# Performance work log

Hardware: AMD Instinct MI355X
Metric: run time of the kernel (lower is better)

## Reference

```python
import jax, jax.numpy as jnp
import numpy as np

VOCAB = 50000
EMB = 32
HID = 32
NUM_CLASSES = 2


def setup_inputs() -> dict:
    key = jax.random.key(0)
    ks = jax.random.split(key, 8)
    B, S = 1024, 512
    x = jax.random.randint(ks[0], (B, S), 0, VOCAB, dtype=jnp.int64)
    # embedding table has vocab_size + 1 rows, per `len(encoder.vocab) + 1`
    emb = jax.random.normal(ks[1], (VOCAB + 1, EMB), dtype=jnp.float32)
    s = 1.0 / np.sqrt(HID)
    w_ih = jax.random.uniform(ks[2], (4 * HID, EMB), jnp.float32, -s, s)
    w_hh = jax.random.uniform(ks[3], (4 * HID, HID), jnp.float32, -s, s)
    b_ih = jax.random.uniform(ks[4], (4 * HID,), jnp.float32, -s, s)
    b_hh = jax.random.uniform(ks[5], (4 * HID,), jnp.float32, -s, s)
    sf = 1.0 / np.sqrt(HID)
    fc_w = jax.random.uniform(ks[6], (NUM_CLASSES, HID), jnp.float32, -sf, sf)
    fc_b = jax.random.uniform(ks[7], (NUM_CLASSES,), jnp.float32, -sf, sf)
    return {"x": x, "emb": emb, "w_ih": w_ih, "w_hh": w_hh,
            "b_ih": b_ih, "b_hh": b_hh, "fc_w": fc_w, "fc_b": fc_b}


def _lstm_last_h(x, emb, w_ih, w_hh, b_ih, b_hh):
    xe = emb[x]                                        # [B, S, EMB]
    # precompute input-to-gate projection for all timesteps: [B, S, 4H]
    xp = jnp.einsum('bse,ge->bsg', xe, w_ih) + (b_ih + b_hh)
    B = x.shape[0]
    h0 = jnp.zeros((B, HID), xp.dtype)
    c0 = jnp.zeros((B, HID), xp.dtype)

    def step(carry, xt):
        h, c = carry
        gates = xt + h @ w_hh.T                        # [B, 4H]
        i, f, g, o = jnp.split(gates, 4, axis=-1)      # PyTorch gate order
        i = jax.nn.sigmoid(i)
        f = jax.nn.sigmoid(f)
        g = jnp.tanh(g)
        o = jax.nn.sigmoid(o)
        c = f * c + i * g
        h = o * jnp.tanh(c)
        return (h, c), None

    (h_n, c_n), _ = jax.lax.scan(step, (h0, c0), jnp.swapaxes(xp, 0, 1))
    return h_n                                          # last-timestep hidden


def reference(x, emb, w_ih, w_hh, b_ih, b_hh, fc_w, fc_b):
    h_last = _lstm_last_h(x, emb, w_ih, w_hh, b_ih, b_hh)
    return h_last @ fc_w.T + fc_b                       # [B, 2]
```

## Files before the change

kernel.cpp:

```cpp
#include <hip/hip_runtime.h>


#define LOG2E 1.44269504088896340736f

typedef float f32x2 __attribute__((ext_vector_type(2)));
typedef unsigned uv2 __attribute__((ext_vector_type(2)));
typedef float f32x16 __attribute__((ext_vector_type(16)));
typedef float f32x32 __attribute__((ext_vector_type(32)));

__device__ __forceinline__ float fast_rcp(float x) { return __builtin_amdgcn_rcpf(x); }
__device__ __forceinline__ float fast_exp2(float x) { return __builtin_amdgcn_exp2f(x); }

__device__ __forceinline__ f32x2 bcast_both(float x) {
    uv2 r = __builtin_amdgcn_permlane32_swap(__float_as_uint(x), __float_as_uint(x),
                                             false, false);
    f32x2 o;
    o.x = __uint_as_float(r.x);
    o.y = __uint_as_float(r.y);
    return o;
}

#define ROTA(V) __int_as_float(__builtin_amdgcn_mov_dpp(__float_as_int(V), 0x13C, 0xF, 0xF, true))
#define ROTB(V) __int_as_float(__builtin_amdgcn_mov_dpp(__float_as_int(V), 0x134, 0xF, 0xF, true))

__global__ __launch_bounds__(64, 1) void build_ptab(
    const float4* __restrict__ emb4, const float4* __restrict__ wih4,
    const float* __restrict__ bih, const float* __restrict__ bhh,
    float2* __restrict__ ptab, int nrows) {
    const int lane = threadIdx.x;

    float w0[32], w1[32];
#pragma unroll
    for (int q = 0; q < 8; ++q) {
        float4 a = wih4[lane * 8 + q];
        float4 b = wih4[(lane + 64) * 8 + q];
        w0[4 * q + 0] = a.x; w0[4 * q + 1] = a.y; w0[4 * q + 2] = a.z; w0[4 * q + 3] = a.w;
        w1[4 * q + 0] = b.x; w1[4 * q + 1] = b.y; w1[4 * q + 2] = b.z; w1[4 * q + 3] = b.w;
    }
    const float bias0 = bih[lane] + bhh[lane];
    const float bias1 = bih[lane + 64] + bhh[lane + 64];
    const float s0 = -LOG2E;
    const float s1 = (lane < 32) ? (2.0f * LOG2E) : (-LOG2E);

    for (int v = blockIdx.x; v < nrows; v += gridDim.x) {
        float a0 = bias0, a1 = bias1;
#pragma unroll
        for (int q = 0; q < 8; ++q) {
            float4 e = emb4[v * 8 + q];
            a0 = fmaf(e.x, w0[4 * q + 0], a0);
            a0 = fmaf(e.y, w0[4 * q + 1], a0);
            a0 = fmaf(e.z, w0[4 * q + 2], a0);
            a0 = fmaf(e.w, w0[4 * q + 3], a0);
            a1 = fmaf(e.x, w1[4 * q + 0], a1);
            a1 = fmaf(e.y, w1[4 * q + 1], a1);
            a1 = fmaf(e.z, w1[4 * q + 2], a1);
            a1 = fmaf(e.w, w1[4 * q + 3], a1);
        }
        ptab[v * 64 + lane] = make_float2(a0 * s0, a1 * s1);
    }
}

#define STEP(P)                                                                \
    do {                                                                       \
        float _a0 = fmaf(h, wI0, (P).x);                                       \
        float _b0 = fmaf(h, wI1, (P).y);                                       \
        float _a1 = 0.0f, _b1 = 0.0f;                                          \
        float _hA = h, _hB = h;                                                \
        _Pragma("unroll") for (int _j = 0; _j < 15; ++_j) {                    \
            _hA = ROTA(_hA);                                                   \
            _a0 = fmaf(_hA, wA0[_j], _a0);                                     \
            _b0 = fmaf(_hA, wA1[_j], _b0);                                     \
            _hB = ROTB(_hB);                                                   \
            _a1 = fmaf(_hB, wB0[_j], _a1);                                     \
            _b1 = fmaf(_hB, wB1[_j], _b1);                                     \
        }                                                                      \
        _hA = ROTA(_hA);                                                       \
        _a0 = fmaf(_hA, wA0[15], _a0);                                         \
        _b0 = fmaf(_hA, wA1[15], _b0);                                         \
        float _A0 = _a0 + _a1;                     \
        float _A1 = _b0 + _b1;                     \
        float _sg = fast_rcp(1.0f + fast_exp2(_A0));           \
        float _r1 = fast_rcp(1.0f + fast_exp2(_A1));           \
        f32x2 _bs = bcast_both(_sg);                \
        f32x2 _br = bcast_both(_r1);               \
        float _ggs = fmaf(-4.0f * LOG2E, _br.x, 2.0f * LOG2E);  \
        cs = fmaf(_bs.y, cs, _bs.x * _ggs);                                    \
        h = _br.y * fmaf(-2.0f, fast_rcp(1.0f + fast_exp2(cs)), 1.0f);         \
    } while (0)

template <bool PTAB>
__global__ __launch_bounds__(64)
__attribute__((amdgpu_waves_per_eu(1, 1)))
void lstm_scan(
    const int* __restrict__ x,
    const float2* __restrict__ ptab,
    const float* __restrict__ emb,
    const float* __restrict__ wih,
    const float* __restrict__ bih,
    const float* __restrict__ bhh,
    const float* __restrict__ whh,
    const float* __restrict__ fcw,
    const float* __restrict__ fcb,
    float* __restrict__ out,
    int S) {
    extern __shared__ int xrow[];
    const int b = blockIdx.x;
    const int lane = threadIdx.x;

    for (int i = lane; i < S + 16; i += 64) xrow[i] = (i < S) ? x[(size_t)b * S + i] : 0;
    __syncthreads();

    const float s0 = -LOG2E;
    const float s1 = (lane < 32) ? (2.0f * LOG2E) : (-LOG2E);

    int dirA, dirB;
    {
        int gA = __builtin_amdgcn_mov_dpp(lane, 0x13C, 0xF, 0xF, true);
        dirA = (gA == ((lane + 1) & 63)) ? 1 : -1;
        int gB = __builtin_amdgcn_mov_dpp(lane, 0x134, 0xF, 0xF, true);
        dirB = (gB == ((lane + 63) & 63)) ? -1 : 1;
    }

    float wI0, wI1;
    f32x16 wA0, wA1, wB0, wB1;
    {
        const int r0 = lane * 32;
        const int r1 = (lane + 64) * 32;
        wI0 = whh[r0 + (lane & 31)] * s0;
        wI1 = whh[r1 + (lane & 31)] * s1;
#pragma unroll
        for (int j = 0; j < 16; ++j) {
            int cA = (lane + dirA * (j + 1)) & 31;
            wA0[j] = whh[r0 + cA] * s0;
            wA1[j] = whh[r1 + cA] * s1;
        }
#pragma unroll
        for (int j = 0; j < 15; ++j) {
            int cB = (lane + dirB * (j + 1)) & 31;
            wB0[j] = whh[r0 + cB] * s0;
            wB1[j] = whh[r1 + cB] * s1;
        }
        wB0[15] = 0.0f;
        wB1[15] = 0.0f;
    }

    float h = 0.0f, cs = 0.0f;

    if constexpr (PTAB) {
        const char* pb = (const char*)ptab + (unsigned)(lane << 3);
        int i0 = xrow[4], i1 = xrow[5], i2 = xrow[6], i3 = xrow[7];
        f32x2 p0 = *(const f32x2*)(pb + ((unsigned)xrow[0] << 9));
        f32x2 p1 = *(const f32x2*)(pb + ((unsigned)xrow[1] << 9));
        f32x2 p2 = *(const f32x2*)(pb + ((unsigned)xrow[2] << 9));
        f32x2 p3 = *(const f32x2*)(pb + ((unsigned)xrow[3] << 9));
        int t = 0;
        for (; t + 8 <= S; t += 4) {
            STEP(p0); p0 = *(const f32x2*)(pb + ((unsigned)i0 << 9)); i0 = xrow[t + 8];
            STEP(p1); p1 = *(const f32x2*)(pb + ((unsigned)i1 << 9)); i1 = xrow[t + 9];
            STEP(p2); p2 = *(const f32x2*)(pb + ((unsigned)i2 << 9)); i2 = xrow[t + 10];
            STEP(p3); p3 = *(const f32x2*)(pb + ((unsigned)i3 << 9)); i3 = xrow[t + 11];
        }
        if (t + 0 < S) STEP(p0);
        if (t + 1 < S) STEP(p1);
        if (t + 2 < S) STEP(p2);
        if (t + 3 < S) STEP(p3);
        if (t + 4 < S) { f32x2 q = *(const f32x2*)(pb + ((unsigned)i0 << 9)); STEP(q); }
        if (t + 5 < S) { f32x2 q = *(const f32x2*)(pb + ((unsigned)i1 << 9)); STEP(q); }
        if (t + 6 < S) { f32x2 q = *(const f32x2*)(pb + ((unsigned)i2 << 9)); STEP(q); }
    } else {
        f32x32 wi0, wi1;
        {
            const float4* wih4 = (const float4*)wih;
#pragma unroll
            for (int q = 0; q < 8; ++q) {
                float4 a = wih4[lane * 8 + q];
                float4 bb = wih4[(lane + 64) * 8 + q];
                wi0[4 * q + 0] = a.x * s0; wi0[4 * q + 1] = a.y * s0;
                wi0[4 * q + 2] = a.z * s0; wi0[4 * q + 3] = a.w * s0;
                wi1[4 * q + 0] = bb.x * s1; wi1[4 * q + 1] = bb.y * s1;
                wi1[4 * q + 2] = bb.z * s1; wi1[4 * q + 3] = bb.w * s1;
            }
        }
        const float bias0 = (bih[lane] + bhh[lane]) * s0;
        const float bias1 = (bih[lane + 64] + bhh[lane + 64]) * s1;
        const float4* emb4 = (const float4*)emb;
        for (int t = 0; t < S; ++t) {
            int idx = xrow[t];
            float a0 = bias0, a1 = bias1;
#pragma unroll
            for (int q = 0; q < 8; ++q) {
                float4 e = emb4[(size_t)idx * 8 + q];
                a0 = fmaf(e.x, wi0[4 * q + 0], a0);
                a0 = fmaf(e.y, wi0[4 * q + 1], a0);
                a0 = fmaf(e.z, wi0[4 * q + 2], a0);
                a0 = fmaf(e.w, wi0[4 * q + 3], a0);
                a1 = fmaf(e.x, wi1[4 * q + 0], a1);
                a1 = fmaf(e.y, wi1[4 * q + 1], a1);
                a1 = fmaf(e.z, wi1[4 * q + 2], a1);
                a1 = fmaf(e.w, wi1[4 * q + 3], a1);
            }
            f32x2 _p; _p.x = a0; _p.y = a1;
            STEP(_p);
        }
    }

    float wv0 = fcw[lane & 31];
    float wv1 = fcw[32 + (lane & 31)];
    float p0v = (lane < 32) ? h * wv0 : 0.0f;
    float p1v = (lane < 32) ? h * wv1 : 0.0f;
#pragma unroll
    for (int m = 32; m >= 1; m >>= 1) {
        p0v += __shfl_xor(p0v, m, 64);
        p1v += __shfl_xor(p1v, m, 64);
    }
    if (lane == 0) {
        out[b * 2 + 0] = p0v + fcb[0];
        out[b * 2 + 1] = p1v + fcb[1];
    }
}

extern "C" void kernel_launch(void* const* d_in, const int* in_sizes, int n_in,
                              void* d_out, int out_size, void* d_ws, size_t ws_size,
                              hipStream_t stream) {
    const int* x = (const int*)d_in[0];
    const float* emb = (const float*)d_in[1];
    const float* wih = (const float*)d_in[2];
    const float* whh = (const float*)d_in[3];
    const float* bih = (const float*)d_in[4];
    const float* bhh = (const float*)d_in[5];
    const float* fcw = (const float*)d_in[6];
    const float* fcb = (const float*)d_in[7];
    float* out = (float*)d_out;

    const int B = out_size / 2;
    const int S = in_sizes[0] / B;
    const int nrows = in_sizes[1] / 32;

    const size_t need = (size_t)nrows * 64 * sizeof(float2);
    const size_t smem = (size_t)(S + 16) * sizeof(int);

    if (ws_size >= need) {
        float2* ptab = (float2*)d_ws;
        int nb = nrows < 8192 ? nrows : 8192;
        build_ptab<<<nb, 64, 0, stream>>>((const float4*)emb, (const float4*)wih,
                                          bih, bhh, ptab, nrows);
        lstm_scan<true><<<B, 64, smem, stream>>>(x, ptab, emb, wih, bih, bhh, whh,
                                                 fcw, fcb, out, S);
    } else {
        lstm_scan<false><<<B, 64, smem, stream>>>(x, nullptr, emb, wih, bih, bhh, whh,
                                                  fcw, fcb, out, S);
    }
}
```

Before: 138.6 us.

## Split hidden-state rotation into four shorter DPP chains using permlane16 swap

The recurrent matvec used two serial DPP rotation chains of about 16 steps each to gather the 32 hidden values. It now uses a permlane16 swap to fetch the value 16 lanes away and runs four interleaved rotation chains of about 8 steps each, with the weights rearranged to match. This shortens the serial dependency chain on the per-timestep critical path. In exchange it adds a cross-lane swap, more accumulators and registers, and a runtime check that works out which half of the swap result each lane should take.

```diff
diff --git a/kernel.cpp b/kernel.cpp
--- a/kernel.cpp
+++ b/kernel.cpp
@@ -5,7 +5,7 @@
 
 typedef float f32x2 __attribute__((ext_vector_type(2)));
 typedef unsigned uv2 __attribute__((ext_vector_type(2)));
-typedef float f32x16 __attribute__((ext_vector_type(16)));
+typedef float f32x8 __attribute__((ext_vector_type(8)));
 typedef float f32x32 __attribute__((ext_vector_type(32)));
 
 __device__ __forceinline__ float fast_rcp(float x) { return __builtin_amdgcn_rcpf(x); }
@@ -18,6 +18,18 @@
     o.x = __uint_as_float(r.x);
     o.y = __uint_as_float(r.y);
     return o;
+}
+
+__device__ __forceinline__ uv2 p16swap(unsigned x) {
+#if __has_builtin(__builtin_amdgcn_permlane16_swap)
+    return __builtin_amdgcn_permlane16_swap(x, x, false, false);
+#else
+    unsigned other = (unsigned)__shfl_xor((int)x, 16, 64);
+    uv2 r;
+    if (threadIdx.x & 16) { r.x = other; r.y = x; }
+    else                  { r.x = x;     r.y = other; }
+    return r;
+#endif
 }
 
 #define ROTA(V) __int_as_float(__builtin_amdgcn_mov_dpp(__float_as_int(V), 0x13C, 0xF, 0xF, true))
@@ -64,21 +76,28 @@
     do {                                                                       \
         float _a0 = fmaf(h, wI0, (P).x);                                       \
         float _b0 = fmaf(h, wI1, (P).y);                                       \
-        float _a1 = 0.0f, _b1 = 0.0f;                                          \
-        float _hA = h, _hB = h;                                                \
-        _Pragma("unroll") for (int _j = 0; _j < 15; ++_j) {                    \
+        uv2 _sw = p16swap(__float_as_uint(h));                                 \
+        float _h16 = __uint_as_float(useX ? _sw.x : _sw.y);                    \
+        float _a1 = 0.f, _b1 = 0.f, _a2 = 0.f, _b2 = 0.f, _a3 = 0.f, _b3 = 0.f;\
+        float _hA = h, _hB = h, _hC = _h16, _hD = _h16;                        \
+        _a0 = fmaf(_h16, C0[0], _a0);                                          \
+        _b0 = fmaf(_h16, C1[0], _b0);                                          \
+        _Pragma("unroll") for (int _j = 0; _j < 7; ++_j) {                     \
             _hA = ROTA(_hA);                                                   \
-            _a0 = fmaf(_hA, wA0[_j], _a0);                                     \
-            _b0 = fmaf(_hA, wA1[_j], _b0);                                     \
+            _a1 = fmaf(_hA, A0[_j], _a1); _b1 = fmaf(_hA, A1[_j], _b1);        \
             _hB = ROTB(_hB);                                                   \
-            _a1 = fmaf(_hB, wB0[_j], _a1);                                     \
-            _b1 = fmaf(_hB, wB1[_j], _b1);                                     \
+            _a2 = fmaf(_hB, B0[_j], _a2); _b2 = fmaf(_hB, B1[_j], _b2);        \
+            _hC = ROTA(_hC);                                                   \
+            _a0 = fmaf(_hC, C0[_j + 1], _a0); _b0 = fmaf(_hC, C1[_j + 1], _b0);\
+            _hD = ROTB(_hD);                                                   \
+            _a3 = fmaf(_hD, D0[_j], _a3); _b3 = fmaf(_hD, D1[_j], _b3);        \
         }                                                                      \
         _hA = ROTA(_hA);                                                       \
-        _a0 = fmaf(_hA, wA0[15], _a0);                                         \
-        _b0 = fmaf(_hA, wA1[15], _b0);                                         \
-        float _A0 = _a0 + _a1;                     \
-        float _A1 = _b0 + _b1;                     \
+        _a1 = fmaf(_hA, A0[7], _a1); _b1 = fmaf(_hA, A1[7], _b1);              \
+        _hB = ROTB(_hB);                                                       \
+        _a2 = fmaf(_hB, B0[7], _a2); _b2 = fmaf(_hB, B1[7], _b2);              \
+        float _A0 = (_a0 + _a1) + (_a2 + _a3);     \
+        float _A1 = (_b0 + _b1) + (_b2 + _b3);     \
         float _sg = fast_rcp(1.0f + fast_exp2(_A0));           \
         float _r1 = fast_rcp(1.0f + fast_exp2(_A1));           \
         f32x2 _bs = bcast_both(_sg);                \
@@ -120,28 +139,40 @@
         int gB = __builtin_amdgcn_mov_dpp(lane, 0x134, 0xF, 0xF, true);
         dirB = (gB == ((lane + 63) & 63)) ? -1 : 1;
     }
+    bool ok16;
+    {
+        uv2 t = p16swap((unsigned)lane);
+        ok16 = (t.x == (unsigned)(lane & ~16));
+    }
+    const bool useX = ((lane & 16) != 0) == ok16;
 
     float wI0, wI1;
-    f32x16 wA0, wA1, wB0, wB1;
+    f32x8 A0, A1, B0, B1, C0, C1, D0, D1;
     {
-        const int r0 = lane * 32;
-        const int r1 = (lane + 64) * 32;
-        wI0 = whh[r0 + (lane & 31)] * s0;
-        wI1 = whh[r1 + (lane & 31)] * s1;
-#pragma unroll
-        for (int j = 0; j < 16; ++j) {
+        const int r0w = lane * 32;
+        const int r1w = (lane + 64) * 32;
+        wI0 = whh[r0w + (lane & 31)] * s0;
+        wI1 = whh[r1w + (lane & 31)] * s1;
+#pragma unroll
+        for (int j = 0; j < 8; ++j) {
             int cA = (lane + dirA * (j + 1)) & 31;
-            wA0[j] = whh[r0 + cA] * s0;
-            wA1[j] = whh[r1 + cA] * s1;
-        }
-#pragma unroll
-        for (int j = 0; j < 15; ++j) {
             int cB = (lane + dirB * (j + 1)) & 31;
-            wB0[j] = whh[r0 + cB] * s0;
-            wB1[j] = whh[r1 + cB] * s1;
-        }
-        wB0[15] = 0.0f;
-        wB1[15] = 0.0f;
+            int cC = (lane + 16 + dirA * j) & 31;
+            A0[j] = whh[r0w + cA] * s0;
+            A1[j] = whh[r1w + cA] * s1;
+            B0[j] = whh[r0w + cB] * s0;
+            B1[j] = whh[r1w + cB] * s1;
+            C0[j] = whh[r0w + cC] * s0;
+            C1[j] = whh[r1w + cC] * s1;
+        }
+#pragma unroll
+        for (int k = 1; k < 8; ++k) {
+            int cD = (lane + 16 + dirB * k) & 31;
+            D0[k - 1] = whh[r0w + cD] * s0;
+            D1[k - 1] = whh[r1w + cD] * s1;
+        }
+        D0[7] = 0.0f;
+        D1[7] = 0.0f;
     }
 
     float h = 0.0f, cs = 0.0f;
```

After: 143.8 us. +3.8%, slower.
